# Performance work log

Hardware: AMD Instinct MI355X
Metric: run time of the kernel (lower is better)

Reference implementation:

```python
import jax, jax.numpy as jnp
import numpy as np

N = 100000        # nodes
E_RAND = 1600000  # random edges (avg degree 16)
D_IN = 64
D_OUT = 64


def setup_inputs() -> dict:
    key = jax.random.key(0)
    k1, k2, k3, k4, k5 = jax.random.split(key, 5)
    x = jax.random.normal(k1, (N, D_IN), dtype=jnp.float32)
    rows = jax.random.randint(k2, (E_RAND,), 0, N)
    cols = jax.random.randint(k3, (E_RAND,), 0, N)
    loops = jnp.arange(N)  # self loops appended at the end (matches remove+add_self_loops order)
    edge_index = jnp.stack([jnp.concatenate([rows, loops]),
                            jnp.concatenate([cols, loops])]).astype(jnp.int64)
    W = (jax.random.normal(k4, (D_IN, D_OUT), dtype=jnp.float32) / np.float32(np.sqrt(D_IN)))
    b = jax.random.normal(k5, (D_OUT,), dtype=jnp.float32) * 0.01
    return {"x": x, "edge_index": edge_index, "W": W, "b": b}


def reference(x, edge_index, W, b):
    row, col = edge_index[0], edge_index[1]
    # lin(x[row]) == (x @ W + b)[row]; transform once then gather (cheaper, same math)
    xl = x @ W + b                      # [N, D_OUT]
    x_i = xl[row]                       # [E, D_OUT] gather by destination
    x_j = xl[col]                       # [E, D_OUT] gather by source
    alpha = jnp.sum(x_i * x_j, axis=-1)  # [E] per-edge score
    alpha = jax.nn.leaky_relu(alpha, negative_slope=0.2)
    # segment-wise softmax over neighborhoods keyed by row
    m = jax.ops.segment_max(alpha, row, num_segments=N)
    m = jnp.where(jnp.isfinite(m), m, 0.0)   # isolated nodes -> -inf max, neutralize
    e = jnp.exp(alpha - m[row])
    s = jax.ops.segment_sum(e, row, num_segments=N)
    alpha = e / (s[row] + 1e-16)
    # dropout(p=0.6) skipped: reference runs in eval mode (deterministic)
    out = jax.ops.segment_sum(x_j * alpha[:, None], row, num_segments=N)  # [N, D_OUT]
    return out
```

## Files before the change

kernel.cpp:

```cpp
#include <hip/hip_runtime.h>
#include <hip/hip_bf16.h>


#define LEAKY_SLOPE 0.2f
#define BK_SHIFT 5
#define BK_NODES 32
#define CAPB 768
#define CH 8192
#define NBP 3136
#define MAXK 8

typedef __attribute__((ext_vector_type(8))) short short8;
typedef __attribute__((ext_vector_type(4))) float f32x4;

struct HiLo { short hi, lo; };

__device__ __forceinline__ HiLo split2(float f) {
    HiLo r;
    unsigned u = __float_as_uint(f);
    r.hi = (short)(u >> 16);
    float fh = __uint_as_float(u & 0xFFFF0000u);
    r.lo = (short)(__float_as_uint(f - fh) >> 16);
    return r;
}

union PreShMem {
    struct { short wt_hi[64 * 72]; short wt_lo[64 * 72]; } lin;
    int hc[NBP];
};

__global__ __launch_bounds__(1024) void k_prelin(const float* __restrict__ x,
                                                 const float* __restrict__ W,
                                                 const float* __restrict__ b,
                                                 const int* __restrict__ row,
                                                 float* __restrict__ xl,
                                                 unsigned short* __restrict__ xlh,
                                                 unsigned short* __restrict__ cntg,
                                                 int N, int E, int NB,
                                                 int ntiles, int nch) {
    __shared__ PreShMem sh;
    int tid = threadIdx.x;

    if ((int)blockIdx.x < nch) {
        for (int i = tid; i < NBP; i += 1024) sh.hc[i] = 0;
        __syncthreads();
        int e0 = (int)blockIdx.x * CH;
        int e1 = min(E, e0 + CH);
        for (int e = e0 + tid; e < e1; e += 1024)
            atomicAdd(&sh.hc[row[e] >> BK_SHIFT], 1);
        __syncthreads();
        unsigned short* orow = cntg + (size_t)blockIdx.x * NBP;
        for (int i = tid; i < NB; i += 1024) orow[i] = (unsigned short)sh.hc[i];
    } else {
        for (int i = tid; i < 4096; i += 1024) {
            int k = i >> 6, n = i & 63;
            HiLo h = split2(W[i]);
            sh.lin.wt_hi[n * 72 + k] = h.hi;
            sh.lin.wt_lo[n * 72 + k] = h.lo;
        }
        __syncthreads();

        int wave = tid >> 6, lane = tid & 63;
        int tile = ((int)blockIdx.x - nch) * 16 + wave;
        if (tile >= ntiles) return;
        int node0 = tile * 16;
        int m = lane & 15;
        int quad = lane >> 4;

        f32x4 acc[4] = {{0.f, 0.f, 0.f, 0.f}, {0.f, 0.f, 0.f, 0.f},
                        {0.f, 0.f, 0.f, 0.f}, {0.f, 0.f, 0.f, 0.f}};

#pragma unroll
        for (int ks = 0; ks < 64; ks += 32) {
            const float* xr = x + (size_t)(node0 + m) * 64 + ks + quad * 8;
            float4 xa = *(const float4*)xr;
            float4 xb = *(const float4*)(xr + 4);
            short8 a_hi, a_lo;
            {
                HiLo h0 = split2(xa.x), h1 = split2(xa.y), h2 = split2(xa.z), h3 = split2(xa.w);
                HiLo h4 = split2(xb.x), h5 = split2(xb.y), h6 = split2(xb.z), h7 = split2(xb.w);
                a_hi[0] = h0.hi; a_lo[0] = h0.lo;  a_hi[1] = h1.hi; a_lo[1] = h1.lo;
                a_hi[2] = h2.hi; a_lo[2] = h2.lo;  a_hi[3] = h3.hi; a_lo[3] = h3.lo;
                a_hi[4] = h4.hi; a_lo[4] = h4.lo;  a_hi[5] = h5.hi; a_lo[5] = h5.lo;
                a_hi[6] = h6.hi; a_lo[6] = h6.lo;  a_hi[7] = h7.hi; a_lo[7] = h7.lo;
            }
#pragma unroll
            for (int g = 0; g < 4; ++g) {
                int n = g * 16 + m;
                int off = n * 72 + ks + quad * 8;
                short8 bh = *(const short8*)&sh.lin.wt_hi[off];
                short8 bl = *(const short8*)&sh.lin.wt_lo[off];
                acc[g] = __builtin_amdgcn_mfma_f32_16x16x32_bf16(a_hi, bh, acc[g], 0, 0, 0);
                acc[g] = __builtin_amdgcn_mfma_f32_16x16x32_bf16(a_lo, bh, acc[g], 0, 0, 0);
                acc[g] = __builtin_amdgcn_mfma_f32_16x16x32_bf16(a_hi, bl, acc[g], 0, 0, 0);
            }
        }

#pragma unroll
        for (int g = 0; g < 4; ++g) {
            float bias = b[g * 16 + m];
#pragma unroll
            for (int r = 0; r < 4; ++r) {
                int node = node0 + quad * 4 + r;
                if (node < N) {
                    float v = acc[g][r] + bias;
                    xl[(size_t)node * 64 + g * 16 + m] = v;
                    xlh[(size_t)node * 64 + g * 16 + m] =
                        (unsigned short)(__float_as_uint(v) >> 16);
                }
            }
        }
    }
}

__global__ __launch_bounds__(256) void k_tot(unsigned short* __restrict__ cntg,
                                             int* __restrict__ tot,
                                             int NB, int nch) {
    int wavegid = (((int)blockIdx.x * 256) + (int)threadIdx.x) >> 6;
    int lane = threadIdx.x & 63;
    int b = wavegid;
    if (b >= NB) return;

    int K = (nch + 63) >> 6;
    int v[MAXK];
    int s = 0;
    int c0 = lane * K;
#pragma unroll
    for (int k = 0; k < MAXK; ++k) {
        if (k < K) {
            int c = c0 + k;
            v[k] = (c < nch) ? (int)cntg[(size_t)c * NBP + b] : 0;
        }
    }
#pragma unroll
    for (int k = 0; k < MAXK; ++k) {
        if (k < K) { int t = v[k]; v[k] = s; s += t; }
    }
    int inc = s;
#pragma unroll
    for (int o = 1; o < 64; o <<= 1) {
        int t = __shfl_up(inc, o, 64);
        if (lane >= o) inc += t;
    }
    int exc = inc - s;
#pragma unroll
    for (int k = 0; k < MAXK; ++k) {
        if (k < K) {
            int c = c0 + k;
            if (c < nch)
                cntg[(size_t)c * NBP + b] = (unsigned short)(v[k] + exc);
        }
    }
    if (lane == 63) tot[b] = inc;
}

__global__ __launch_bounds__(1024) void k_base(const int* __restrict__ tot,
                                               int* __restrict__ base,
                                               int NB, int E) {
    __shared__ int segsum[16];
    int tid = threadIdx.x, lane = tid & 63, wid = tid >> 6;
    int segbeg = tid * 4;
    int loc[4];
    int s = 0;
#pragma unroll
    for (int k = 0; k < 4; ++k) {
        int i = segbeg + k;
        int t = (i < NB) ? tot[i] : 0;
        loc[k] = s; s += t;
    }
    int v = s;
#pragma unroll
    for (int o = 1; o < 64; o <<= 1) {
        int t = __shfl_up(v, o, 64);
        if (lane >= o) v += t;
    }
    if (lane == 63) segsum[wid] = v;
    __syncthreads();
    int woff = 0;
#pragma unroll
    for (int w = 0; w < 16; ++w) woff += (w < wid) ? segsum[w] : 0;
    int segoff = (v - s) + woff;
#pragma unroll
    for (int k = 0; k < 4; ++k) {
        int i = segbeg + k;
        if (i < NB) base[i] = loc[k] + segoff;
    }
    if (tid == 0) base[NB] = E;
}

__global__ __launch_bounds__(1024) void k_scat(const int* __restrict__ row,
                                               const int* __restrict__ col,
                                               const unsigned short* __restrict__ cntg,
                                               const int* __restrict__ base,
                                               unsigned* __restrict__ slab,
                                               int E, int NB, int nch) {
    __shared__ int pfx[NBP];
    __shared__ int pos[NBP];
    int tid = threadIdx.x;
    int cb = (int)blockIdx.x;
    int chunk = (nch % 8 == 0) ? (cb % 8) * (nch / 8) + cb / 8 : cb;

    const unsigned short* crow = cntg + (size_t)chunk * NBP;
    for (int i = tid; i < NB; i += 1024) {
        pfx[i] = base[i] + (int)crow[i];
        pos[i] = 0;
    }
    __syncthreads();

    int e0 = chunk * CH;
    int e1 = min(E, e0 + CH);
    for (int e = e0 + tid; e < e1; e += 1024) {
        int r = row[e], c = col[e];
        int bkt = r >> BK_SHIFT;
        int rank = atomicAdd(&pos[bkt], 1);
        slab[pfx[bkt] + rank] =
            ((unsigned)(r & (BK_NODES - 1)) << 17) | (unsigned)c;
    }
}

template <int CTRL>
__device__ __forceinline__ float dpp_add(float x) {
    int y = __builtin_amdgcn_update_dpp(0, __float_as_int(x), CTRL, 0xF, 0xF, true);
    return x + __int_as_float(y);
}

__device__ __forceinline__ float red8(float d) {
    d = dpp_add<0xB1>(d);
    d = dpp_add<0x4E>(d);
    d = dpp_add<0x141>(d);
    return d;
}

__device__ __forceinline__ void bf8_to_f8(uint4 u, float4& a, float4& b) {
    a.x = __uint_as_float(u.x << 16);
    a.y = __uint_as_float(u.x & 0xFFFF0000u);
    a.z = __uint_as_float(u.y << 16);
    a.w = __uint_as_float(u.y & 0xFFFF0000u);
    b.x = __uint_as_float(u.z << 16);
    b.y = __uint_as_float(u.z & 0xFFFF0000u);
    b.z = __uint_as_float(u.w << 16);
    b.w = __uint_as_float(u.w & 0xFFFF0000u);
}

__device__ __forceinline__ float dot4(float4 a, float4 b) {
    return a.x * b.x + a.y * b.y + a.z * b.z + a.w * b.w;
}

__device__ __forceinline__ void edge_upd(int c, uint4 u, int node, float m,
                                         float4 xia, float4 xib,
                                         float& l, float4& A, float4& B) {
    float4 xa, xb;
    bf8_to_f8(u, xa, xb);
    float d = red8(dot4(xia, xa) + dot4(xib, xb));
    d = fmaxf(d, LEAKY_SLOPE * d);
    float p = __expf(d - m);
    p = (c != node) ? p : 0.0f;
    l += p;
    A.x += p * xa.x; A.y += p * xa.y; A.z += p * xa.z; A.w += p * xa.w;
    B.x += p * xb.x; B.y += p * xb.y; B.z += p * xb.z; B.w += p * xb.w;
}

__global__ __launch_bounds__(256) void k_agg(const float* __restrict__ xl,
                                             const unsigned short* __restrict__ xlh,
                                             const unsigned* __restrict__ slab,
                                             const int* __restrict__ base,
                                             float* __restrict__ out, int N) {
    __shared__ int raw[CAPB];
    __shared__ int colsh[CAPB];
    __shared__ int deg[BK_NODES], sc[BK_NODES], cur[BK_NODES], ord[BK_NODES];

    int bkt = blockIdx.x;
    int tid = threadIdx.x;

    int s0 = base[bkt];
    int cnt = base[bkt + 1] - s0;
    if (cnt > CAPB) cnt = CAPB;

    if (tid < BK_NODES) { deg[tid] = 0; cur[tid] = 0; }
    __syncthreads();

    const unsigned* sl = slab + s0;
    for (int i = tid; i < cnt; i += 256) {
        int e = (int)sl[i];
        raw[i] = e;
        atomicAdd(&deg[((unsigned)e) >> 17], 1);
    }
    __syncthreads();

    if (tid < BK_NODES) {
        int d = deg[tid];
        int v = d;
#pragma unroll
        for (int o = 1; o < 32; o <<= 1) {
            int t = __shfl_up(v, o, 32);
            if (tid >= o) v += t;
        }
        sc[tid] = v;
        int r = 0;
#pragma unroll
        for (int j = 0; j < BK_NODES; ++j) {
            int dj = deg[j];
            r += (dj > d) || (dj == d && j < tid);
        }
        ord[r] = tid;
    }
    __syncthreads();

    for (int i = tid; i < cnt; i += 256) {
        unsigned pk = (unsigned)raw[i];
        int rl = pk >> 17;
        int p = sc[rl] - deg[rl] + atomicAdd(&cur[rl], 1);
        colsh[p] = (int)(pk & 0x1FFFFu);
    }
    __syncthreads();

    int grp = tid >> 3;
    int g = tid & 7;
    const uint4* xh4 = (const uint4*)xlh;
    int n0 = ord[grp];
    int node = bkt * BK_NODES + n0;
    if (node < N) {
        int beg = sc[n0] - deg[n0];
        int end = sc[n0];
        float4 xia = ((const float4*)xl)[(size_t)node * 16 + 2 * g];
        float4 xib = ((const float4*)xl)[(size_t)node * 16 + 2 * g + 1];

        float m = red8(dot4(xia, xia) + dot4(xib, xib));
        float l = 1.0f;
        float4 accA = xia;
        float4 accB = xib;

        int e = beg;
        for (; e + 6 <= end; e += 6) {
            int c0 = colsh[e],     c1 = colsh[e + 1], c2 = colsh[e + 2];
            int c3 = colsh[e + 3], c4 = colsh[e + 4], c5 = colsh[e + 5];
            uint4 u0 = xh4[(unsigned)(c0 * 8 + g)];
            uint4 u1 = xh4[(unsigned)(c1 * 8 + g)];
            uint4 u2 = xh4[(unsigned)(c2 * 8 + g)];
            uint4 u3 = xh4[(unsigned)(c3 * 8 + g)];
            uint4 u4 = xh4[(unsigned)(c4 * 8 + g)];
            uint4 u5 = xh4[(unsigned)(c5 * 8 + g)];
            edge_upd(c0, u0, node, m, xia, xib, l, accA, accB);
            edge_upd(c1, u1, node, m, xia, xib, l, accA, accB);
            edge_upd(c2, u2, node, m, xia, xib, l, accA, accB);
            edge_upd(c3, u3, node, m, xia, xib, l, accA, accB);
            edge_upd(c4, u4, node, m, xia, xib, l, accA, accB);
            edge_upd(c5, u5, node, m, xia, xib, l, accA, accB);
        }
        for (; e + 2 <= end; e += 2) {
            int c0 = colsh[e], c1 = colsh[e + 1];
            uint4 u0 = xh4[(unsigned)(c0 * 8 + g)];
            uint4 u1 = xh4[(unsigned)(c1 * 8 + g)];
            edge_upd(c0, u0, node, m, xia, xib, l, accA, accB);
            edge_upd(c1, u1, node, m, xia, xib, l, accA, accB);
        }
        for (; e < end; ++e) {
            int c = colsh[e];
            uint4 u = xh4[(unsigned)(c * 8 + g)];
            edge_upd(c, u, node, m, xia, xib, l, accA, accB);
        }
        float inv = 1.0f / l;
        float4 oA = {accA.x * inv, accA.y * inv, accA.z * inv, accA.w * inv};
        float4 oB = {accB.x * inv, accB.y * inv, accB.z * inv, accB.w * inv};
        ((float4*)out)[(size_t)node * 16 + 2 * g] = oA;
        ((float4*)out)[(size_t)node * 16 + 2 * g + 1] = oB;
    }
}

extern "C" void kernel_launch(void* const* d_in, const int* in_sizes, int n_in,
                              void* d_out, int out_size, void* d_ws, size_t ws_size,
                              hipStream_t stream) {
    const float* x = (const float*)d_in[0];
    const int* ei = (const int*)d_in[1];
    const float* W = (const float*)d_in[2];
    const float* b = (const float*)d_in[3];

    const int N = in_sizes[0] / 64;
    const int E = in_sizes[1] / 2;
    const int NO = N * 64;
    const int NB = (N + BK_NODES - 1) >> BK_SHIFT;
    const int NCH = (E + CH - 1) / CH;
    const int* row = ei;
    const int* col = ei + E;

    float* out = (float*)d_out;

    float* ws = (float*)d_ws;
    float* xl           = ws;
    unsigned short* xlh = (unsigned short*)(xl + (size_t)NO);
    unsigned short* cntg= xlh + (size_t)NO;
    int* tot            = (int*)(cntg + (size_t)NCH * NBP);
    int* base           = tot + NB;
    unsigned* slab      = (unsigned*)(base + NB + 1);

    const int ntiles = (N + 15) / 16;
    const int lblocks = (ntiles + 15) / 16;

    k_prelin<<<NCH + lblocks, 1024, 0, stream>>>(x, W, b, row, xl, xlh,
                                                 cntg, N, E, NB, ntiles, NCH);
    k_tot<<<(NB + 3) / 4, 256, 0, stream>>>(cntg, tot, NB, NCH);
    k_base<<<1, 1024, 0, stream>>>(tot, base, NB, E);
    k_scat<<<NCH, 1024, 0, stream>>>(row, col, cntg, base, slab, E, NB, NCH);
    k_agg<<<NB, 256, 0, stream>>>(xl, xlh, slab, base, out, N);
}
```

Baseline: 163.7 us.

## Fuse linear transform into scatter kernel and pad per-node edge lists to six

Moves the x@W+b MFMA tile work from the histogram kernel into the scatter kernel, so the linear blocks run alongside edge scattering instead of histogramming. In the aggregation kernel, each node's edge list is padded up to a multiple of six with self-index entries, which enables a single software-pipelined loop that prefetches the next six gathers while processing the current ones. It also raises the shared capacity CAPB and adds an occupancy hint to launch_bounds. Padding adds duplicate self-edges, which is only correct if edge_upd skips entries equal to the node itself. It also raises per-block shared memory.

```diff
diff --git a/kernel.cpp b/kernel.cpp
--- a/kernel.cpp
+++ b/kernel.cpp
@@ -5,7 +5,7 @@
 #define LEAKY_SLOPE 0.2f
 #define BK_SHIFT 5
 #define BK_NODES 32
-#define CAPB 768
+#define CAPB 960
 #define CH 8192
 #define NBP 3136
 #define MAXK 8
@@ -24,33 +24,137 @@
     return r;
 }
 
-union PreShMem {
+__global__ __launch_bounds__(1024) void k_hist(const int* __restrict__ row,
+                                               unsigned short* __restrict__ cntg,
+                                               int E, int NB) {
+    __shared__ int hc[NBP];
+    int tid = threadIdx.x;
+    for (int i = tid; i < NBP; i += 1024) hc[i] = 0;
+    __syncthreads();
+    int e0 = (int)blockIdx.x * CH;
+    int e1 = min(E, e0 + CH);
+    for (int e = e0 + tid; e < e1; e += 1024)
+        atomicAdd(&hc[row[e] >> BK_SHIFT], 1);
+    __syncthreads();
+    unsigned short* orow = cntg + (size_t)blockIdx.x * NBP;
+    for (int i = tid; i < NB; i += 1024) orow[i] = (unsigned short)hc[i];
+}
+
+__global__ __launch_bounds__(256) void k_tot(unsigned short* __restrict__ cntg,
+                                             int* __restrict__ tot,
+                                             int NB, int nch) {
+    int wavegid = (((int)blockIdx.x * 256) + (int)threadIdx.x) >> 6;
+    int lane = threadIdx.x & 63;
+    int b = wavegid;
+    if (b >= NB) return;
+
+    int K = (nch + 63) >> 6;
+    int v[MAXK];
+    int s = 0;
+    int c0 = lane * K;
+#pragma unroll
+    for (int k = 0; k < MAXK; ++k) {
+        if (k < K) {
+            int c = c0 + k;
+            v[k] = (c < nch) ? (int)cntg[(size_t)c * NBP + b] : 0;
+        }
+    }
+#pragma unroll
+    for (int k = 0; k < MAXK; ++k) {
+        if (k < K) { int t = v[k]; v[k] = s; s += t; }
+    }
+    int inc = s;
+#pragma unroll
+    for (int o = 1; o < 64; o <<= 1) {
+        int t = __shfl_up(inc, o, 64);
+        if (lane >= o) inc += t;
+    }
+    int exc = inc - s;
+#pragma unroll
+    for (int k = 0; k < MAXK; ++k) {
+        if (k < K) {
+            int c = c0 + k;
+            if (c < nch)
+                cntg[(size_t)c * NBP + b] = (unsigned short)(v[k] + exc);
+        }
+    }
+    if (lane == 63) tot[b] = inc;
+}
+
+__global__ __launch_bounds__(1024) void k_base(const int* __restrict__ tot,
+                                               int* __restrict__ base,
+                                               int NB, int E) {
+    __shared__ int segsum[16];
+    int tid = threadIdx.x, lane = tid & 63, wid = tid >> 6;
+    int segbeg = tid * 4;
+    int loc[4];
+    int s = 0;
+#pragma unroll
+    for (int k = 0; k < 4; ++k) {
+        int i = segbeg + k;
+        int t = (i < NB) ? tot[i] : 0;
+        loc[k] = s; s += t;
+    }
+    int v = s;
+#pragma unroll
+    for (int o = 1; o < 64; o <<= 1) {
+        int t = __shfl_up(v, o, 64);
+        if (lane >= o) v += t;
+    }
+    if (lane == 63) segsum[wid] = v;
+    __syncthreads();
+    int woff = 0;
+#pragma unroll
+    for (int w = 0; w < 16; ++w) woff += (w < wid) ? segsum[w] : 0;
+    int segoff = (v - s) + woff;
+#pragma unroll
+    for (int k = 0; k < 4; ++k) {
+        int i = segbeg + k;
+        if (i < NB) base[i] = loc[k] + segoff;
+    }
+    if (tid == 0) base[NB] = E;
+}
+
+union SLShMem {
     struct { short wt_hi[64 * 72]; short wt_lo[64 * 72]; } lin;
-    int hc[NBP];
+    struct { int pfx[NBP], pos[NBP]; } sc;
 };
 
-__global__ __launch_bounds__(1024) void k_prelin(const float* __restrict__ x,
-                                                 const float* __restrict__ W,
-                                                 const float* __restrict__ b,
-                                                 const int* __restrict__ row,
-                                                 float* __restrict__ xl,
-                                                 unsigned short* __restrict__ xlh,
-                                                 unsigned short* __restrict__ cntg,
-                                                 int N, int E, int NB,
-                                                 int ntiles, int nch) {
-    __shared__ PreShMem sh;
+__global__ __launch_bounds__(1024) void k_scatlin(const float* __restrict__ x,
+                                                  const float* __restrict__ W,
+                                                  const float* __restrict__ b,
+                                                  const int* __restrict__ row,
+                                                  const int* __restrict__ col,
+                                                  float* __restrict__ xl,
+                                                  unsigned short* __restrict__ xlh,
+                                                  const unsigned short* __restrict__ cntg,
+                                                  const int* __restrict__ base,
+                                                  unsigned* __restrict__ slab,
+                                                  int N, int E, int NB,
+                                                  int ntiles, int nsc, int nch) {
+    __shared__ SLShMem sh;
     int tid = threadIdx.x;
 
-    if ((int)blockIdx.x < nch) {
-        for (int i = tid; i < NBP; i += 1024) sh.hc[i] = 0;
+    if ((int)blockIdx.x < nsc) {
+        int cb = (int)blockIdx.x;
+        int chunk = (nch % 8 == 0) ? (cb % 8) * (nch / 8) + cb / 8 : cb;
+
+        const unsigned short* crow = cntg + (size_t)chunk * NBP;
+        for (int i = tid; i < NB; i += 1024) {
+            sh.sc.pfx[i] = base[i] + (int)crow[i];
+            sh.sc.pos[i] = 0;
+        }
         __syncthreads();
-        int e0 = (int)blockIdx.x * CH;
+
+        int e0 = chunk * CH;
         int e1 = min(E, e0 + CH);
-        for (int e = e0 + tid; e < e1; e += 1024)
-            atomicAdd(&sh.hc[row[e] >> BK_SHIFT], 1);
-        __syncthreads();
-        unsigned short* orow = cntg + (size_t)blockIdx.x * NBP;
-        for (int i = tid; i < NB; i += 1024) orow[i] = (unsigned short)sh.hc[i];
+        for (int e = e0 + tid; e < e1; e += 1024) {
+            int r = row[e], c = col[e];
+            int bkt = r >> BK_SHIFT;
+            int rank = atomicAdd(&sh.sc.pos[bkt], 1);
+            slab[sh.sc.pfx[bkt] + rank] =
+                ((unsigned)(r & (BK_NODES - 1)) << 17) | (unsigned)c;
+        }
     } else {
         for (int i = tid; i < 4096; i += 1024) {
             int k = i >> 6, n = i & 63;
@@ -61,7 +165,7 @@
         __syncthreads();
 
         int wave = tid >> 6, lane = tid & 63;
-        int tile = ((int)blockIdx.x - nch) * 16 + wave;
+        int tile = ((int)blockIdx.x - nsc) * 16 + wave;
         if (tile >= ntiles) return;
         int node0 = tile * 16;
         int m = lane & 15;
@@ -113,111 +217,6 @@
     }
 }
 
-__global__ __launch_bounds__(256) void k_tot(unsigned short* __restrict__ cntg,
-                                             int* __restrict__ tot,
-                                             int NB, int nch) {
-    int wavegid = (((int)blockIdx.x * 256) + (int)threadIdx.x) >> 6;
-    int lane = threadIdx.x & 63;
-    int b = wavegid;
-    if (b >= NB) return;
-
-    int K = (nch + 63) >> 6;
-    int v[MAXK];
-    int s = 0;
-    int c0 = lane * K;
-#pragma unroll
-    for (int k = 0; k < MAXK; ++k) {
-        if (k < K) {
-            int c = c0 + k;
-            v[k] = (c < nch) ? (int)cntg[(size_t)c * NBP + b] : 0;
-        }
-    }
-#pragma unroll
-    for (int k = 0; k < MAXK; ++k) {
-        if (k < K) { int t = v[k]; v[k] = s; s += t; }
-    }
-    int inc = s;
-#pragma unroll
-    for (int o = 1; o < 64; o <<= 1) {
-        int t = __shfl_up(inc, o, 64);
-        if (lane >= o) inc += t;
-    }
-    int exc = inc - s;
-#pragma unroll
-    for (int k = 0; k < MAXK; ++k) {
-        if (k < K) {
-            int c = c0 + k;
-            if (c < nch)
-                cntg[(size_t)c * NBP + b] = (unsigned short)(v[k] + exc);
-        }
-    }
-    if (lane == 63) tot[b] = inc;
-}
-
-__global__ __launch_bounds__(1024) void k_base(const int* __restrict__ tot,
-                                               int* __restrict__ base,
-                                               int NB, int E) {
-    __shared__ int segsum[16];
-    int tid = threadIdx.x, lane = tid & 63, wid = tid >> 6;
-    int segbeg = tid * 4;
-    int loc[4];
-    int s = 0;
-#pragma unroll
-    for (int k = 0; k < 4; ++k) {
-        int i = segbeg + k;
-        int t = (i < NB) ? tot[i] : 0;
-        loc[k] = s; s += t;
-    }
-    int v = s;
-#pragma unroll
-    for (int o = 1; o < 64; o <<= 1) {
-        int t = __shfl_up(v, o, 64);
-        if (lane >= o) v += t;
-    }
-    if (lane == 63) segsum[wid] = v;
-    __syncthreads();
-    int woff = 0;
-#pragma unroll
-    for (int w = 0; w < 16; ++w) woff += (w < wid) ? segsum[w] : 0;
-    int segoff = (v - s) + woff;
-#pragma unroll
-    for (int k = 0; k < 4; ++k) {
-        int i = segbeg + k;
-        if (i < NB) base[i] = loc[k] + segoff;
-    }
-    if (tid == 0) base[NB] = E;
-}
-
-__global__ __launch_bounds__(1024) void k_scat(const int* __restrict__ row,
-                                               const int* __restrict__ col,
-                                               const unsigned short* __restrict__ cntg,
-                                               const int* __restrict__ base,
-                                               unsigned* __restrict__ slab,
-                                               int E, int NB, int nch) {
-    __shared__ int pfx[NBP];
-    __shared__ int pos[NBP];
-    int tid = threadIdx.x;
-    int cb = (int)blockIdx.x;
-    int chunk = (nch % 8 == 0) ? (cb % 8) * (nch / 8) + cb / 8 : cb;
-
-    const unsigned short* crow = cntg + (size_t)chunk * NBP;
-    for (int i = tid; i < NB; i += 1024) {
-        pfx[i] = base[i] + (int)crow[i];
-        pos[i] = 0;
-    }
-    __syncthreads();
-
-    int e0 = chunk * CH;
-    int e1 = min(E, e0 + CH);
-    for (int e = e0 + tid; e < e1; e += 1024) {
-        int r = row[e], c = col[e];
-        int bkt = r >> BK_SHIFT;
-        int rank = atomicAdd(&pos[bkt], 1);
-        slab[pfx[bkt] + rank] =
-            ((unsigned)(r & (BK_NODES - 1)) << 17) | (unsigned)c;
-    }
-}
-
 template <int CTRL>
 __device__ __forceinline__ float dpp_add(float x) {
     int y = __builtin_amdgcn_update_dpp(0, __float_as_int(x), CTRL, 0xF, 0xF, true);
@@ -260,14 +259,15 @@
     B.x += p * xb.x; B.y += p * xb.y; B.z += p * xb.z; B.w += p * xb.w;
 }
 
-__global__ __launch_bounds__(256) void k_agg(const float* __restrict__ xl,
-                                             const unsigned short* __restrict__ xlh,
-                                             const unsigned* __restrict__ slab,
-                                             const int* __restrict__ base,
-                                             float* __restrict__ out, int N) {
+__global__ __launch_bounds__(256, 8) void k_agg(const float* __restrict__ xl,
+                                                const unsigned short* __restrict__ xlh,
+                                                const unsigned* __restrict__ slab,
+                                                const int* __restrict__ base,
+                                                float* __restrict__ out, int N) {
     __shared__ int raw[CAPB];
     __shared__ int colsh[CAPB];
-    __shared__ int deg[BK_NODES], sc[BK_NODES], cur[BK_NODES], ord[BK_NODES];
+    __shared__ int deg[BK_NODES], degp[BK_NODES], sc[BK_NODES];
+    __shared__ int cur[BK_NODES], ord[BK_NODES];
 
     int bkt = blockIdx.x;
     int tid = threadIdx.x;
@@ -289,7 +289,9 @@
 
     if (tid < BK_NODES) {
         int d = deg[tid];
-        int v = d;
+        int dp = ((d + 5) / 6) * 6;
+        degp[tid] = dp;
+        int v = dp;
 #pragma unroll
         for (int o = 1; o < 32; o <<= 1) {
             int t = __shfl_up(v, o, 32);
@@ -309,8 +311,14 @@
     for (int i = tid; i < cnt; i += 256) {
         unsigned pk = (unsigned)raw[i];
         int rl = pk >> 17;
-        int p = sc[rl] - deg[rl] + atomicAdd(&cur[rl], 1);
+        int p = sc[rl] - degp[rl] + atomicAdd(&cur[rl], 1);
         colsh[p] = (int)(pk & 0x1FFFFu);
+    }
+    if (tid < BK_NODES) {
+        int b0 = sc[tid] - degp[tid] + deg[tid];
+        int b1 = sc[tid];
+        int selfid = bkt * BK_NODES + tid;
+        for (int i = b0; i < b1; ++i) colsh[i] = selfid;
     }
     __syncthreads();
 
@@ -320,45 +328,46 @@
     int n0 = ord[grp];
     int node = bkt * BK_NODES + n0;
     if (node < N) {
-        int beg = sc[n0] - deg[n0];
+        int e = sc[n0] - degp[n0];
         int end = sc[n0];
         float4 xia = ((const float4*)xl)[(size_t)node * 16 + 2 * g];
         float4 xib = ((const float4*)xl)[(size_t)node * 16 + 2 * g + 1];
 
-        float m = red8(dot4(xia, xia) + dot4(xib, xib));
+        float mval = red8(dot4(xia, xia) + dot4(xib, xib));
         float l = 1.0f;
         float4 accA = xia;
         float4 accB = xib;
 
-        int e = beg;
-        for (; e + 6 <= end; e += 6) {
-            int c0 = colsh[e],     c1 = colsh[e + 1], c2 = colsh[e + 2];
-            int c3 = colsh[e + 3], c4 = colsh[e + 4], c5 = colsh[e + 5];
-            uint4 u0 = xh4[(unsigned)(c0 * 8 + g)];
-            uint4 u1 = xh4[(unsigned)(c1 * 8 + g)];
-            uint4 u2 = xh4[(unsigned)(c2 * 8 + g)];
-            uint4 u3 = xh4[(unsigned)(c3 * 8 + g)];
-            uint4 u4 = xh4[(unsigned)(c4 * 8 + g)];
-            uint4 u5 = xh4[(unsigned)(c5 * 8 + g)];
-            edge_upd(c0, u0, node, m, xia, xib, l, accA, accB);
-            edge_upd(c1, u1, node, m, xia, xib, l, accA, accB);
-            edge_upd(c2, u2, node, m, xia, xib, l, accA, accB);
-            edge_upd(c3, u3, node, m, xia, xib, l, accA, accB);
-            edge_upd(c4, u4, node, m, xia, xib, l, accA, accB);
-            edge_upd(c5, u5, node, m, xia, xib, l, accA, accB);
-        }
-        for (; e + 2 <= end; e += 2) {
-            int c0 = colsh[e], c1 = colsh[e + 1];
-            uint4 u0 = xh4[(unsigned)(c0 * 8 + g)];
-            uint4 u1 = xh4[(unsigned)(c1 * 8 + g)];
-            edge_upd(c0, u0, node, m, xia, xib, l, accA, accB);
-            edge_upd(c1, u1, node, m, xia, xib, l, accA, accB);
-        }
-        for (; e < end; ++e) {
-            int c = colsh[e];
-            uint4 u = xh4[(unsigned)(c * 8 + g)];
-            edge_upd(c, u, node, m, xia, xib, l, accA, accB);
-        }
+        int c0 = colsh[e],     c1 = colsh[e + 1], c2 = colsh[e + 2];
+        int c3 = colsh[e + 3], c4 = colsh[e + 4], c5 = colsh[e + 5];
+        uint4 u0 = xh4[(unsigned)(c0 * 8 + g)];
+        uint4 u1 = xh4[(unsigned)(c1 * 8 + g)];
+        uint4 u2 = xh4[(unsigned)(c2 * 8 + g)];
+        uint4 u3 = xh4[(unsigned)(c3 * 8 + g)];
+        uint4 u4 = xh4[(unsigned)(c4 * 8 + g)];
+        uint4 u5 = xh4[(unsigned)(c5 * 8 + g)];
+
+        for (; e + 12 <= end; e += 6) {
+            edge_upd(c0, u0, node, mval, xia, xib, l, accA, accB);
+            c0 = colsh[e + 6];  u0 = xh4[(unsigned)(c0 * 8 + g)];
+            edge_upd(c1, u1, node, mval, xia, xib, l, accA, accB);
+            c1 = colsh[e + 7];  u1 = xh4[(unsigned)(c1 * 8 + g)];
+            edge_upd(c2, u2, node, mval, xia, xib, l, accA, accB);
+            c2 = colsh[e + 8];  u2 = xh4[(unsigned)(c2 * 8 + g)];
+            edge_upd(c3, u3, node, mval, xia, xib, l, accA, accB);
+            c3 = colsh[e + 9];  u3 = xh4[(unsigned)(c3 * 8 + g)];
+            edge_upd(c4, u4, node, mval, xia, xib, l, accA, accB);
+            c4 = colsh[e + 10]; u4 = xh4[(unsigned)(c4 * 8 + g)];
+            edge_upd(c5, u5, node, mval, xia, xib, l, accA, accB);
+            c5 = colsh[e + 11]; u5 = xh4[(unsigned)(c5 * 8 + g)];
+        }
+        edge_upd(c0, u0, node, mval, xia, xib, l, accA, accB);
+        edge_upd(c1, u1, node, mval, xia, xib, l, accA, accB);
+        edge_upd(c2, u2, node, mval, xia, xib, l, accA, accB);
+        edge_upd(c3, u3, node, mval, xia, xib, l, accA, accB);
+        edge_upd(c4, u4, node, mval, xia, xib, l, accA, accB);
+        edge_upd(c5, u5, node, mval, xia, xib, l, accA, accB);
+
         float inv = 1.0f / l;
         float4 oA = {accA.x * inv, accA.y * inv, accA.z * inv, accA.w * inv};
         float4 oB = {accB.x * inv, accB.y * inv, accB.z * inv, accB.w * inv};
@@ -396,10 +405,11 @@
     const int ntiles = (N + 15) / 16;
     const int lblocks = (ntiles + 15) / 16;
 
-    k_prelin<<<NCH + lblocks, 1024, 0, stream>>>(x, W, b, row, xl, xlh,
-                                                 cntg, N, E, NB, ntiles, NCH);
+    k_hist<<<NCH, 1024, 0, stream>>>(row, cntg, E, NB);
     k_tot<<<(NB + 3) / 4, 256, 0, stream>>>(cntg, tot, NB, NCH);
     k_base<<<1, 1024, 0, stream>>>(tot, base, NB, E);
-    k_scat<<<NCH, 1024, 0, stream>>>(row, col, cntg, base, slab, E, NB, NCH);
+    k_scatlin<<<NCH + lblocks, 1024, 0, stream>>>(x, W, b, row, col, xl, xlh,
+                                                  cntg, base, slab,
+                                                  N, E, NB, ntiles, NCH, NCH);
     k_agg<<<NB, 256, 0, stream>>>(xl, xlh, slab, base, out, N);
 }
```

Measured after the change: 294.3 us. 1.8x slower.
